# Kernel tuning notes

Measured on AMD Instinct MI355X. Metric: run time of the kernel, lower is better.

The kernel has to match this reference:

```python
import jax, jax.numpy as jnp
import numpy as np

NUM_LAYERS = 12
AGENT_LEN = 10
EMBED = 768
TEXT_DIM = 512
N_TOK = 1024   # h*w patches
BATCH = 32
N_CLS = 150
N_CTX = 77


def setup_inputs() -> dict:
    key = jax.random.key(0)
    ks = jax.random.split(key, 12)
    s = 0.02
    return {
        "output": jax.random.normal(ks[0], (N_TOK + 1, BATCH, EMBED), jnp.float32),
        "text_feat": jax.random.normal(ks[1], (1, N_CLS, N_CTX, TEXT_DIM), jnp.float32),
        "agent": jax.random.uniform(ks[2], (NUM_LAYERS, AGENT_LEN, EMBED), jnp.float32, -0.05, 0.05),
        "agent_scale": jnp.float32(0.001),
        "w1": jax.random.normal(ks[3], (EMBED, EMBED), jnp.float32) * s,
        "b1": jnp.zeros((EMBED,), jnp.float32),
        "w2": jax.random.normal(ks[4], (EMBED, EMBED), jnp.float32) * s,
        "b2": jnp.zeros((EMBED,), jnp.float32),
        "wm": jax.random.normal(ks[5], (EMBED, EMBED), jnp.float32) * s,
        "bm": jnp.zeros((EMBED,), jnp.float32),
        "wt": jax.random.normal(ks[6], (EMBED, TEXT_DIM), jnp.float32) * s,
        "bt": jnp.zeros((EMBED,), jnp.float32),
        "layer": 0,
    }


def _mask_pool(x, m, wm, bm):
    # x: [b, n, d], m: [b, n, a] -> [b, a, d]
    w = jax.nn.sigmoid(m)
    pooled = jnp.einsum('bna,bnd->bad', w, x) / (w.sum(axis=1)[:, :, None] + 1e-6)
    return pooled @ wm.T + bm


def reference(output, text_feat, agent, agent_scale, w1, b1, w2, b2, wm, bm, wt, bt, layer):
    cls_tok, x = output[:1], output[1:]          # [1,b,d], [n,b,d]
    n, b, d = x.shape
    scale = d ** (-0.5)

    # agent tokens for this layer, broadcast to batch
    ag = jnp.broadcast_to(agent[layer], (b, agent.shape[1], d))   # [b,a,d]

    # proj_text: mean over ctx tokens, l2-normalize, linear+relu
    tf = text_feat.mean(axis=-2)                                   # [1,c,text_dim]
    tf = tf / jnp.linalg.norm(tf, axis=-1, keepdims=True)
    temb = jax.nn.relu(tf @ wt.T + bt)                             # [1,c,d]
    temb = jnp.broadcast_to(temb, (b,) + temb.shape[1:])           # [b,c,d]

    feats = x.transpose(1, 0, 2)                                   # [b,n,d]

    # agent_mask
    masked_text = _mask_pool(temb, jnp.einsum('bad,bcd->bca', ag, temb) * scale, wm, bm)
    masked_vis = _mask_pool(feats, jnp.einsum('bnd,bad->bna', feats, ag) * scale, wm, bm)
    ag2 = ag + masked_text + masked_vis                            # [b,a,d]

    # agent_attention: agent <- text
    attn_t = jax.nn.softmax(jnp.einsum('bad,bcd->bac', ag2, temb) * scale, axis=-1)
    v = jnp.einsum('bac,bcd->bad', attn_t, temb) @ w1.T + b1       # [b,a,d]

    # feats <- agent
    attn_v = jax.nn.softmax(jnp.einsum('bnd,bad->bna', feats, ag2) * scale, axis=-1)
    delta = jnp.einsum('bna,bad->bnd', attn_v, v) @ w2.T + b2      # [b,n,d]

    x = x + delta.transpose(1, 0, 2) * agent_scale
    return jnp.concatenate([cls_tok, x], axis=0)
```

## Files before the change

kernel.cpp:

```cpp
#include <hip/hip_runtime.h>
#include <hip/hip_bf16.h>
#include <math.h>

#define BB 32
#define DD 768
#define AL 10
#define NC 150
#define CTX 77
#define TD 512
#define SCALE 0.036084391824351615f
#define CHUNKS 32
#define ROWS_PB 32

__global__ void k_tp1(const float* __restrict__ tfeat, float* __restrict__ tpart) {
    int c = blockIdx.x, qq = blockIdx.y;
    int t = threadIdx.x;
    int j0 = qq * 20, j1 = (qq == 3) ? CTX : j0 + 20;
    const float* base = tfeat + (size_t)c * CTX * TD;
    float s0 = 0.f, s1 = 0.f;
    for (int j = j0; j < j1; ++j) {
        s0 += base[j * TD + t];
        s1 += base[j * TD + t + 256];
    }
    tpart[((size_t)c * 4 + qq) * TD + t] = s0;
    tpart[((size_t)c * 4 + qq) * TD + t + 256] = s1;
}

__global__ void k_tp2(const float* __restrict__ tpart, float* __restrict__ tfn) {
    int c = blockIdx.x, t = threadIdx.x;
    float s0 = 0.f, s1 = 0.f;
    for (int q = 0; q < 4; ++q) {
        s0 += tpart[((size_t)c * 4 + q) * TD + t];
        s1 += tpart[((size_t)c * 4 + q) * TD + t + 256];
    }
    s0 *= (1.f / CTX); s1 *= (1.f / CTX);
    __shared__ float red[256];
    red[t] = s0 * s0 + s1 * s1;
    __syncthreads();
    for (int o = 128; o > 0; o >>= 1) { if (t < o) red[t] += red[t + o]; __syncthreads(); }
    float rn = rsqrtf(red[0]);
    tfn[c * TD + t] = s0 * rn;
    tfn[c * TD + t + 256] = s1 * rn;
}

__global__ void k_temb(const float* __restrict__ tfn, const float* __restrict__ wt,
                       const float* __restrict__ bt, float* __restrict__ temb) {
    int c = blockIdx.x, dch = blockIdx.y;
    int t = threadIdx.x;
    __shared__ float row[TD];
    row[t] = tfn[(size_t)c * TD + t];
    row[t + 256] = tfn[(size_t)c * TD + t + 256];
    __syncthreads();
    int d = dch * 256 + t;
    const float* wr = wt + (size_t)d * TD;
    float acc = bt[d];
    for (int k = 0; k < TD; k += 4) {
        float4 w4 = *reinterpret_cast<const float4*>(wr + k);
        acc += row[k] * w4.x + row[k + 1] * w4.y + row[k + 2] * w4.z + row[k + 3] * w4.w;
    }
    temb[(size_t)c * DD + d] = fmaxf(acc, 0.f);
}

__global__ void k_wtext(const float* __restrict__ temb, const float* __restrict__ agent,
                        const int* __restrict__ layerp, float* __restrict__ wtex) {
    int c = blockIdx.x / AL, a = blockIdx.x % AL;
    int l = threadIdx.x;
    const float* ar = agent + ((size_t)layerp[0] * AL + a) * DD;
    const float* tr = temb + (size_t)c * DD;
    float p = 0.f;
    for (int j = 0; j < 12; ++j) { int d = j * 64 + l; p += ar[d] * tr[d]; }
    #pragma unroll
    for (int o = 1; o < 64; o <<= 1) p += __shfl_xor(p, o);
    if (l == 0) wtex[c * AL + a] = 1.f / (1.f + __expf(-p * SCALE));
}

__global__ void k_ptext(const float* __restrict__ temb, const float* __restrict__ wtex,
                        float* __restrict__ ptex) {
    int a = blockIdx.x / 3, dch = blockIdx.x % 3;
    int d = dch * 256 + threadIdx.x;
    float num = 0.f, den = 0.f;
    for (int c = 0; c < NC; ++c) {
        float wv = wtex[c * AL + a];
        num += wv * temb[(size_t)c * DD + d];
        den += wv;
    }
    ptex[(size_t)a * DD + d] = num / (den + 1e-6f);
}

__global__ void k_mtextB10(const float* __restrict__ ptex, const float* __restrict__ wm,
                           const float* __restrict__ bm, const float* __restrict__ agent,
                           const int* __restrict__ layerp, float* __restrict__ B10) {
    int a = blockIdx.x, dch = blockIdx.y;
    int t = threadIdx.x;
    __shared__ float row[DD];
    for (int i = t; i < DD; i += 256) row[i] = ptex[(size_t)a * DD + i];
    __syncthreads();
    int d = dch * 256 + t;
    const float* wr = wm + (size_t)d * DD;
    float acc = 0.f;
    for (int k = 0; k < DD; k += 4) {
        float4 w4 = *reinterpret_cast<const float4*>(wr + k);
        acc += row[k] * w4.x + row[k + 1] * w4.y + row[k + 2] * w4.z + row[k + 3] * w4.w;
    }
    B10[(size_t)a * DD + d] = acc + bm[d] + agent[((size_t)layerp[0] * AL + a) * DD + d];
}

__global__ __launch_bounds__(256, 2)
void k_pass1(const float* __restrict__ outp, const float* __restrict__ agent,
             const int* __restrict__ layerp, __hip_bfloat16* __restrict__ num_bf,
             float* __restrict__ den_part) {
    int chunk = blockIdx.x, b = blockIdx.y;
    int tid = threadIdx.x, lane = tid & 63, w = tid >> 6;
    __shared__ float agl[AL * DD];
    __shared__ float xs[8][DD];
    __shared__ float wl[ROWS_PB][AL];
    const float* ab = agent + (size_t)layerp[0] * AL * DD;
    for (int i = tid; i < AL * DD; i += 256) agl[i] = ab[i];
    float acc0[AL], acc1[AL], acc2[AL];
    #pragma unroll
    for (int a = 0; a < AL; ++a) { acc0[a] = 0.f; acc1[a] = 0.f; acc2[a] = 0.f; }
    __syncthreads();
    for (int g = 0; g < 4; ++g) {
        int la = w * 2, lb = la + 1;
        int ga = g * 8 + la, gb = ga + 1;
        const float* pA = outp + ((size_t)(1 + chunk * ROWS_PB + ga) * BB + b) * DD + lane * 4;
        const float* pB = pA + (size_t)BB * DD;
        float4 xa0 = *(const float4*)(pA);
        float4 xa1 = *(const float4*)(pA + 256);
        float4 xa2 = *(const float4*)(pA + 512);
        float4 xb0 = *(const float4*)(pB);
        float4 xb1 = *(const float4*)(pB + 256);
        float4 xb2 = *(const float4*)(pB + 512);
        *(float4*)(&xs[la][lane * 4])       = xa0;
        *(float4*)(&xs[la][lane * 4 + 256]) = xa1;
        *(float4*)(&xs[la][lane * 4 + 512]) = xa2;
        *(float4*)(&xs[lb][lane * 4])       = xb0;
        *(float4*)(&xs[lb][lane * 4 + 256]) = xb1;
        *(float4*)(&xs[lb][lane * 4 + 512]) = xb2;
        #pragma unroll
        for (int a = 0; a < AL; ++a) {
            const float* agc = agl + a * DD + lane * 4;
            float4 c0 = *(const float4*)(agc);
            float4 c1 = *(const float4*)(agc + 256);
            float4 c2 = *(const float4*)(agc + 512);
            float pa = xa0.x*c0.x + xa0.y*c0.y + xa0.z*c0.z + xa0.w*c0.w
                     + xa1.x*c1.x + xa1.y*c1.y + xa1.z*c1.z + xa1.w*c1.w
                     + xa2.x*c2.x + xa2.y*c2.y + xa2.z*c2.z + xa2.w*c2.w;
            float pb = xb0.x*c0.x + xb0.y*c0.y + xb0.z*c0.z + xb0.w*c0.w
                     + xb1.x*c1.x + xb1.y*c1.y + xb1.z*c1.z + xb1.w*c1.w
                     + xb2.x*c2.x + xb2.y*c2.y + xb2.z*c2.z + xb2.w*c2.w;
            #pragma unroll
            for (int o = 1; o < 64; o <<= 1) { pa += __shfl_xor(pa, o); pb += __shfl_xor(pb, o); }
            if (lane == a) {
                wl[ga][a] = 1.f / (1.f + __expf(-pa * SCALE));
                wl[gb][a] = 1.f / (1.f + __expf(-pb * SCALE));
            }
        }
        __syncthreads();
        #pragma unroll
        for (int row = 0; row < 8; ++row) {
            float x0 = xs[row][tid], x1 = xs[row][tid + 256], x2 = xs[row][tid + 512];
            int rw = g * 8 + row;
            #pragma unroll
            for (int a = 0; a < AL; ++a) {
                float wg = wl[rw][a];
                acc0[a] += wg * x0; acc1[a] += wg * x1; acc2[a] += wg * x2;
            }
        }
        __syncthreads();
    }
    __hip_bfloat16* np_ = num_bf + ((size_t)b * CHUNKS + chunk) * AL * DD;
    #pragma unroll
    for (int a = 0; a < AL; ++a) {
        np_[a * DD + tid]       = __float2bfloat16(acc0[a]);
        np_[a * DD + tid + 256] = __float2bfloat16(acc1[a]);
        np_[a * DD + tid + 512] = __float2bfloat16(acc2[a]);
    }
    if (tid < AL) {
        float dn = 0.f;
        for (int rw = 0; rw < ROWS_PB; ++rw) dn += wl[rw][tid];
        den_part[((size_t)b * CHUNKS + chunk) * AL + tid] = dn;
    }
}

__global__ void k_poolvis(const __hip_bfloat16* __restrict__ num_bf,
                          const float* __restrict__ den_part, float* __restrict__ pvis) {
    int idx = blockIdx.x;
    int a = idx % AL, b = idx / AL;
    int t = threadIdx.x;
    float den = 0.f;
    for (int c = 0; c < CHUNKS; ++c) den += den_part[((size_t)b * CHUNKS + c) * AL + a];
    float inv = 1.f / (den + 1e-6f);
    for (int dd = 0; dd < 3; ++dd) {
        int d = dd * 256 + t;
        float num = 0.f;
        for (int c = 0; c < CHUNKS; ++c)
            num += __bfloat162float(num_bf[((size_t)b * CHUNKS + c) * AL * DD + a * DD + d]);
        pvis[((size_t)b * AL + a) * DD + d] = num * inv;
    }
}

__global__ __launch_bounds__(256)
void k_gemmsk(const float* __restrict__ A, const float* __restrict__ W,
              float* __restrict__ part) {
    int n0 = blockIdx.x * 64, m0 = blockIdx.y * 64, k0 = blockIdx.z * 192;
    int tid = threadIdx.x;
    int tx = tid % 16, ty = tid / 16;
    __shared__ float As[64][36];
    __shared__ float Ws[64][36];
    float acc[4][4] = {};
    for (int kk = 0; kk < 192; kk += 32) {
        #pragma unroll
        for (int s = 0; s < 2; ++s) {
            int i = s * 256 + tid;
            int r = i >> 3, c4 = (i & 7) * 4;
            float4 av = *reinterpret_cast<const float4*>(A + (size_t)(m0 + r) * DD + k0 + kk + c4);
            float4 wv = *reinterpret_cast<const float4*>(W + (size_t)(n0 + r) * DD + k0 + kk + c4);
            *reinterpret_cast<float4*>(&As[r][c4]) = av;
            *reinterpret_cast<float4*>(&Ws[r][c4]) = wv;
        }
        __syncthreads();
        #pragma unroll
        for (int k4 = 0; k4 < 32; k4 += 4) {
            float4 a[4], wv[4];
            #pragma unroll
            for (int i = 0; i < 4; ++i) a[i] = *reinterpret_cast<const float4*>(&As[ty * 4 + i][k4]);
            #pragma unroll
            for (int j = 0; j < 4; ++j) wv[j] = *reinterpret_cast<const float4*>(&Ws[tx * 4 + j][k4]);
            #pragma unroll
            for (int i = 0; i < 4; ++i)
                #pragma unroll
                for (int j = 0; j < 4; ++j)
                    acc[i][j] += a[i].x * wv[j].x + a[i].y * wv[j].y
                               + a[i].z * wv[j].z + a[i].w * wv[j].w;
        }
        __syncthreads();
    }
    float* pb = part + (size_t)blockIdx.z * 320 * DD;
    #pragma unroll
    for (int i = 0; i < 4; ++i) {
        int m = m0 + ty * 4 + i;
        #pragma unroll
        for (int j = 0; j < 4; ++j)
            pb[(size_t)m * DD + n0 + tx * 4 + j] = acc[i][j];
    }
}

__global__ void k_gemmred(const float* __restrict__ part, const float* __restrict__ bias,
                          const float* __restrict__ brow, float* __restrict__ dst) {
    int m = blockIdx.x, t = threadIdx.x;
    int a = m % AL;
    for (int dd = 0; dd < 3; ++dd) {
        int d = dd * 256 + t;
        float v = part[(size_t)m * DD + d]
                + part[(size_t)320 * DD + (size_t)m * DD + d]
                + part[(size_t)2 * 320 * DD + (size_t)m * DD + d]
                + part[(size_t)3 * 320 * DD + (size_t)m * DD + d];
        v += bias[d];
        if (brow) v += brow[(size_t)a * DD + d];
        dst[(size_t)m * DD + d] = v;
    }
}

__global__ void k_tattn(const float* __restrict__ ag2, const float* __restrict__ temb,
                        float* __restrict__ u) {
    int a = blockIdx.x, b = blockIdx.y;
    int t = threadIdx.x;
    __shared__ float q[DD];
    __shared__ float p[NC];
    __shared__ float red[256];
    const float* qb = ag2 + ((size_t)b * AL + a) * DD;
    for (int i = t; i < DD; i += 256) q[i] = qb[i];
    __syncthreads();
    float myp = -1e30f;
    if (t < NC) {
        const float* tr = temb + (size_t)t * DD;
        float s = 0.f;
        for (int k = 0; k < DD; k += 4) {
            float4 t4 = *reinterpret_cast<const float4*>(tr + k);
            s += q[k] * t4.x + q[k + 1] * t4.y + q[k + 2] * t4.z + q[k + 3] * t4.w;
        }
        myp = s * SCALE;
    }
    red[t] = myp; __syncthreads();
    for (int o = 128; o > 0; o >>= 1) { if (t < o) red[t] = fmaxf(red[t], red[t + o]); __syncthreads(); }
    float mx = red[0]; __syncthreads();
    float e = (t < NC) ? __expf(myp - mx) : 0.f;
    red[t] = e; __syncthreads();
    for (int o = 128; o > 0; o >>= 1) { if (t < o) red[t] += red[t + o]; __syncthreads(); }
    float inv = 1.f / red[0];
    if (t < NC) p[t] = e * inv;
    __syncthreads();
    float u0 = 0.f, u1 = 0.f, u2 = 0.f;
    for (int c = 0; c < NC; ++c) {
        const float* tr = temb + (size_t)c * DD;
        float pc = p[c];
        u0 += pc * tr[t]; u1 += pc * tr[t + 256]; u2 += pc * tr[t + 512];
    }
    float* ur = u + ((size_t)b * AL + a) * DD;
    ur[t] = u0; ur[t + 256] = u1; ur[t + 512] = u2;
}

__global__ __launch_bounds__(256, 2)
void k_pass2(const float* __restrict__ outp, const float* __restrict__ ag2,
             const float* __restrict__ v2, const float* __restrict__ ascale,
             float* __restrict__ out) {
    int chunk = blockIdx.x, b = blockIdx.y;
    int tid = threadIdx.x, lane = tid & 63, w = tid >> 6;
    __shared__ float agl[AL * DD];
    __shared__ float xs[8][DD];
    __shared__ float pl[8][AL];
    float vr0[AL], vr1[AL], vr2[AL];
    #pragma unroll
    for (int a = 0; a < AL; ++a) {
        const float* vrow = v2 + ((size_t)b * AL + a) * DD;
        vr0[a] = vrow[tid]; vr1[a] = vrow[tid + 256]; vr2[a] = vrow[tid + 512];
    }
    const float* ab = ag2 + (size_t)b * AL * DD;
    for (int i = tid; i < AL * DD; i += 256) agl[i] = ab[i];
    float asc = ascale[0];
    __syncthreads();
    for (int g = 0; g < 4; ++g) {
        int la = w * 2, lb = la + 1;
        int ga = g * 8 + la, gb = ga + 1;
        const float* pA = outp + ((size_t)(1 + chunk * ROWS_PB + ga) * BB + b) * DD + lane * 4;
        const float* pB = pA + (size_t)BB * DD;
        float4 xa0 = *(const float4*)(pA);
        float4 xa1 = *(const float4*)(pA + 256);
        float4 xa2 = *(const float4*)(pA + 512);
        float4 xb0 = *(const float4*)(pB);
        float4 xb1 = *(const float4*)(pB + 256);
        float4 xb2 = *(const float4*)(pB + 512);
        *(float4*)(&xs[la][lane * 4])       = xa0;
        *(float4*)(&xs[la][lane * 4 + 256]) = xa1;
        *(float4*)(&xs[la][lane * 4 + 512]) = xa2;
        *(float4*)(&xs[lb][lane * 4])       = xb0;
        *(float4*)(&xs[lb][lane * 4 + 256]) = xb1;
        *(float4*)(&xs[lb][lane * 4 + 512]) = xb2;
        float sA[AL], sB[AL];
        #pragma unroll
        for (int a = 0; a < AL; ++a) {
            const float* agc = agl + a * DD + lane * 4;
            float4 c0 = *(const float4*)(agc);
            float4 c1 = *(const float4*)(agc + 256);
            float4 c2 = *(const float4*)(agc + 512);
            float pa = xa0.x*c0.x + xa0.y*c0.y + xa0.z*c0.z + xa0.w*c0.w
                     + xa1.x*c1.x + xa1.y*c1.y + xa1.z*c1.z + xa1.w*c1.w
                     + xa2.x*c2.x + xa2.y*c2.y + xa2.z*c2.z + xa2.w*c2.w;
            float pb = xb0.x*c0.x + xb0.y*c0.y + xb0.z*c0.z + xb0.w*c0.w
                     + xb1.x*c1.x + xb1.y*c1.y + xb1.z*c1.z + xb1.w*c1.w
                     + xb2.x*c2.x + xb2.y*c2.y + xb2.z*c2.z + xb2.w*c2.w;
            #pragma unroll
            for (int o = 1; o < 64; o <<= 1) { pa += __shfl_xor(pa, o); pb += __shfl_xor(pb, o); }
            sA[a] = pa * SCALE; sB[a] = pb * SCALE;
        }
        float mA = sA[0], mB = sB[0];
        #pragma unroll
        for (int a = 1; a < AL; ++a) { mA = fmaxf(mA, sA[a]); mB = fmaxf(mB, sB[a]); }
        float ZA = 0.f, ZB = 0.f;
        #pragma unroll
        for (int a = 0; a < AL; ++a) {
            sA[a] = __expf(sA[a] - mA); ZA += sA[a];
            sB[a] = __expf(sB[a] - mB); ZB += sB[a];
        }
        float iA = asc / ZA, iB = asc / ZB;
        #pragma unroll
        for (int a = 0; a < AL; ++a) {
            if (lane == a) { pl[la][a] = sA[a] * iA; pl[lb][a] = sB[a] * iB; }
        }
        __syncthreads();
        #pragma unroll
        for (int row = 0; row < 8; ++row) {
            float x0 = xs[row][tid], x1 = xs[row][tid + 256], x2 = xs[row][tid + 512];
            float d0 = 0.f, d1 = 0.f, d2 = 0.f;
            #pragma unroll
            for (int a = 0; a < AL; ++a) {
                float pa = pl[row][a];
                d0 += pa * vr0[a]; d1 += pa * vr1[a]; d2 += pa * vr2[a];
            }
            float* orow = out + ((size_t)(1 + chunk * ROWS_PB + g * 8 + row) * BB + b) * DD;
            orow[tid]       = x0 + d0;
            orow[tid + 256] = x1 + d1;
            orow[tid + 512] = x2 + d2;
        }
        __syncthreads();
    }
}

extern "C" void kernel_launch(void* const* d_in, const int* in_sizes, int n_in,
                              void* d_out, int out_size, void* d_ws, size_t ws_size,
                              hipStream_t stream) {
    const float* outp   = (const float*)d_in[0];
    const float* tfeat  = (const float*)d_in[1];
    const float* agent  = (const float*)d_in[2];
    const float* ascale = (const float*)d_in[3];
    const float* w1 = (const float*)d_in[4];
    const float* b1 = (const float*)d_in[5];
    const float* w2 = (const float*)d_in[6];
    const float* b2 = (const float*)d_in[7];
    const float* wm = (const float*)d_in[8];
    const float* bm = (const float*)d_in[9];
    const float* wt = (const float*)d_in[10];
    const float* bt = (const float*)d_in[11];
    const int* layerp = (const int*)d_in[12];
    float* out = (float*)d_out;

    float* ws = (float*)d_ws;
    float* tfn   = ws;
    float* temb  = tfn + NC * TD;
    float* wtex  = temb + NC * DD;
    float* ptex  = wtex + NC * AL;
    float* B10   = ptex + AL * DD;
    float* pvis  = B10 + AL * DD;
    float* ag2   = pvis + BB * AL * DD;
    float* u     = ag2 + BB * AL * DD;
    float* v     = u + BB * AL * DD;
    float* v2    = v + BB * AL * DD;
    float* den_part = v2 + BB * AL * DD;
    __hip_bfloat16* num_bf = (__hip_bfloat16*)(den_part + BB * CHUNKS * AL);
    float* tpart = u;
    float* part  = (float*)num_bf;

    hipMemcpyAsync(out, outp, (size_t)BB * DD * sizeof(float),
                   hipMemcpyDeviceToDevice, stream);

    k_pass1<<<dim3(CHUNKS, BB), 256, 0, stream>>>(outp, agent, layerp, num_bf, den_part);
    k_tp1<<<dim3(NC, 4), 256, 0, stream>>>(tfeat, tpart);
    k_tp2<<<NC, 256, 0, stream>>>(tpart, tfn);
    k_temb<<<dim3(NC, 3), 256, 0, stream>>>(tfn, wt, bt, temb);
    k_wtext<<<NC * AL, 64, 0, stream>>>(temb, agent, layerp, wtex);
    k_ptext<<<30, 256, 0, stream>>>(temb, wtex, ptex);
    k_mtextB10<<<dim3(AL, 3), 256, 0, stream>>>(ptex, wm, bm, agent, layerp, B10);
    k_poolvis<<<BB * AL, 256, 0, stream>>>(num_bf, den_part, pvis);
    k_gemmsk<<<dim3(12, 5, 4), 256, 0, stream>>>(pvis, wm, part);
    k_gemmred<<<320, 256, 0, stream>>>(part, bm, B10, ag2);
    k_tattn<<<dim3(AL, BB), 256, 0, stream>>>(ag2, temb, u);
    k_gemmsk<<<dim3(12, 5, 4), 256, 0, stream>>>(u, w1, part);
    k_gemmred<<<320, 256, 0, stream>>>(part, b1, nullptr, v);
    k_gemmsk<<<dim3(12, 5, 4), 256, 0, stream>>>(v, w2, part);
    k_gemmred<<<320, 256, 0, stream>>>(part, b2, nullptr, v2);
    k_pass2<<<dim3(CHUNKS, BB), 256, 0, stream>>>(outp, ag2, v2, ascale, out);
}
```

Measured before the change: 478.9 us.

## Fuse text-path kernels, fold split-K reductions into consumers, drop smem staging in passes

The text projection path is collapsed from six kernels to three: the split context sum is merged into one kernel, the agent-text dot products are fused into the temb projection via shared and global atomics, and pooling is fused with the wm GEMV. The separate split-K reduction kernels are removed; consumers (tattn, pass2, and a new GEMM that sums partials plus bias while loading A) add the four partial slices directly. k_pass1 and k_pass2 no longer stage rows in shared memory, re-reading x from global in a second loop, and their occupancy hint rises from 2 to 4. This cuts launches and intermediate traffic but re-reads the large activation tensor and duplicates partial-sum work across blocks.

```diff
diff --git a/kernel.cpp b/kernel.cpp
--- a/kernel.cpp
+++ b/kernel.cpp
@@ -11,27 +11,16 @@
 #define SCALE 0.036084391824351615f
 #define CHUNKS 32
 #define ROWS_PB 32
-
-__global__ void k_tp1(const float* __restrict__ tfeat, float* __restrict__ tpart) {
-    int c = blockIdx.x, qq = blockIdx.y;
-    int t = threadIdx.x;
-    int j0 = qq * 20, j1 = (qq == 3) ? CTX : j0 + 20;
+#define PS ((size_t)320 * DD)
+
+__global__ void k_tp(const float* __restrict__ tfeat, float* __restrict__ tfn) {
+    int c = blockIdx.x, t = threadIdx.x;
     const float* base = tfeat + (size_t)c * CTX * TD;
     float s0 = 0.f, s1 = 0.f;
-    for (int j = j0; j < j1; ++j) {
+    #pragma unroll 4
+    for (int j = 0; j < CTX; ++j) {
         s0 += base[j * TD + t];
         s1 += base[j * TD + t + 256];
-    }
-    tpart[((size_t)c * 4 + qq) * TD + t] = s0;
-    tpart[((size_t)c * 4 + qq) * TD + t + 256] = s1;
-}
-
-__global__ void k_tp2(const float* __restrict__ tpart, float* __restrict__ tfn) {
-    int c = blockIdx.x, t = threadIdx.x;
-    float s0 = 0.f, s1 = 0.f;
-    for (int q = 0; q < 4; ++q) {
-        s0 += tpart[((size_t)c * 4 + q) * TD + t];
-        s1 += tpart[((size_t)c * 4 + q) * TD + t + 256];
     }
     s0 *= (1.f / CTX); s1 *= (1.f / CTX);
     __shared__ float red[256];
@@ -44,12 +33,16 @@
 }
 
 __global__ void k_temb(const float* __restrict__ tfn, const float* __restrict__ wt,
-                       const float* __restrict__ bt, float* __restrict__ temb) {
+                       const float* __restrict__ bt, const float* __restrict__ agent,
+                       const int* __restrict__ layerp, float* __restrict__ temb,
+                       float* __restrict__ wtex_raw) {
     int c = blockIdx.x, dch = blockIdx.y;
-    int t = threadIdx.x;
+    int t = threadIdx.x, lane = t & 63;
     __shared__ float row[TD];
+    __shared__ float wsum[16];
     row[t] = tfn[(size_t)c * TD + t];
     row[t + 256] = tfn[(size_t)c * TD + t + 256];
+    if (t < 16) wsum[t] = 0.f;
     __syncthreads();
     int d = dch * 256 + t;
     const float* wr = wt + (size_t)d * TD;
@@ -58,72 +51,70 @@
         float4 w4 = *reinterpret_cast<const float4*>(wr + k);
         acc += row[k] * w4.x + row[k + 1] * w4.y + row[k + 2] * w4.z + row[k + 3] * w4.w;
     }
-    temb[(size_t)c * DD + d] = fmaxf(acc, 0.f);
-}
-
-__global__ void k_wtext(const float* __restrict__ temb, const float* __restrict__ agent,
-                        const int* __restrict__ layerp, float* __restrict__ wtex) {
-    int c = blockIdx.x / AL, a = blockIdx.x % AL;
-    int l = threadIdx.x;
-    const float* ar = agent + ((size_t)layerp[0] * AL + a) * DD;
-    const float* tr = temb + (size_t)c * DD;
-    float p = 0.f;
-    for (int j = 0; j < 12; ++j) { int d = j * 64 + l; p += ar[d] * tr[d]; }
-    #pragma unroll
-    for (int o = 1; o < 64; o <<= 1) p += __shfl_xor(p, o);
-    if (l == 0) wtex[c * AL + a] = 1.f / (1.f + __expf(-p * SCALE));
-}
-
-__global__ void k_ptext(const float* __restrict__ temb, const float* __restrict__ wtex,
-                        float* __restrict__ ptex) {
-    int a = blockIdx.x / 3, dch = blockIdx.x % 3;
-    int d = dch * 256 + threadIdx.x;
-    float num = 0.f, den = 0.f;
-    for (int c = 0; c < NC; ++c) {
-        float wv = wtex[c * AL + a];
-        num += wv * temb[(size_t)c * DD + d];
-        den += wv;
-    }
-    ptex[(size_t)a * DD + d] = num / (den + 1e-6f);
-}
-
-__global__ void k_mtextB10(const float* __restrict__ ptex, const float* __restrict__ wm,
-                           const float* __restrict__ bm, const float* __restrict__ agent,
-                           const int* __restrict__ layerp, float* __restrict__ B10) {
+    float tv = fmaxf(acc, 0.f);
+    temb[(size_t)c * DD + d] = tv;
+    const float* ag = agent + (size_t)layerp[0] * AL * DD + d;
+    #pragma unroll
+    for (int a = 0; a < AL; ++a) {
+        float p = tv * ag[(size_t)a * DD];
+        #pragma unroll
+        for (int o = 1; o < 64; o <<= 1) p += __shfl_xor(p, o);
+        if (lane == 0) atomicAdd(&wsum[a], p);
+    }
+    __syncthreads();
+    if (t < AL) atomicAdd(&wtex_raw[c * AL + t], wsum[t]);
+}
+
+__global__ void k_text2(const float* __restrict__ temb, const float* __restrict__ wtex_raw,
+                        const float* __restrict__ wm, const float* __restrict__ bm,
+                        const float* __restrict__ agent, const int* __restrict__ layerp,
+                        float* __restrict__ B10) {
     int a = blockIdx.x, dch = blockIdx.y;
     int t = threadIdx.x;
-    __shared__ float row[DD];
-    for (int i = t; i < DD; i += 256) row[i] = ptex[(size_t)a * DD + i];
+    __shared__ float pooled[DD];
+    __shared__ float wv[NC];
+    __shared__ float red[256];
+    float myw = 0.f;
+    if (t < NC) { myw = 1.f / (1.f + __expf(-wtex_raw[t * AL + a] * SCALE)); wv[t] = myw; }
+    red[t] = myw;
+    __syncthreads();
+    for (int o = 128; o > 0; o >>= 1) { if (t < o) red[t] += red[t + o]; __syncthreads(); }
+    float inv = 1.f / (red[0] + 1e-6f);
+    float p0 = 0.f, p1 = 0.f, p2 = 0.f;
+    #pragma unroll 2
+    for (int c = 0; c < NC; ++c) {
+        float wc = wv[c];
+        const float* tr = temb + (size_t)c * DD;
+        p0 += wc * tr[t]; p1 += wc * tr[t + 256]; p2 += wc * tr[t + 512];
+    }
+    pooled[t] = p0 * inv; pooled[t + 256] = p1 * inv; pooled[t + 512] = p2 * inv;
     __syncthreads();
     int d = dch * 256 + t;
     const float* wr = wm + (size_t)d * DD;
     float acc = 0.f;
     for (int k = 0; k < DD; k += 4) {
         float4 w4 = *reinterpret_cast<const float4*>(wr + k);
-        acc += row[k] * w4.x + row[k + 1] * w4.y + row[k + 2] * w4.z + row[k + 3] * w4.w;
+        acc += pooled[k] * w4.x + pooled[k + 1] * w4.y + pooled[k + 2] * w4.z + pooled[k + 3] * w4.w;
     }
     B10[(size_t)a * DD + d] = acc + bm[d] + agent[((size_t)layerp[0] * AL + a) * DD + d];
 }
 
-__global__ __launch_bounds__(256, 2)
+__global__ __launch_bounds__(256, 4)
 void k_pass1(const float* __restrict__ outp, const float* __restrict__ agent,
              const int* __restrict__ layerp, __hip_bfloat16* __restrict__ num_bf,
              float* __restrict__ den_part) {
     int chunk = blockIdx.x, b = blockIdx.y;
     int tid = threadIdx.x, lane = tid & 63, w = tid >> 6;
     __shared__ float agl[AL * DD];
-    __shared__ float xs[8][DD];
     __shared__ float wl[ROWS_PB][AL];
     const float* ab = agent + (size_t)layerp[0] * AL * DD;
     for (int i = tid; i < AL * DD; i += 256) agl[i] = ab[i];
-    float acc0[AL], acc1[AL], acc2[AL];
-    #pragma unroll
-    for (int a = 0; a < AL; ++a) { acc0[a] = 0.f; acc1[a] = 0.f; acc2[a] = 0.f; }
-    __syncthreads();
-    for (int g = 0; g < 4; ++g) {
-        int la = w * 2, lb = la + 1;
-        int ga = g * 8 + la, gb = ga + 1;
-        const float* pA = outp + ((size_t)(1 + chunk * ROWS_PB + ga) * BB + b) * DD + lane * 4;
+    __syncthreads();
+    const float4* agl4 = reinterpret_cast<const float4*>(agl);
+    #pragma unroll
+    for (int pr = 0; pr < 4; ++pr) {
+        int ra = w * 8 + pr * 2, rb = ra + 1;
+        const float* pA = outp + ((size_t)(1 + chunk * ROWS_PB + ra) * BB + b) * DD + lane * 4;
         const float* pB = pA + (size_t)BB * DD;
         float4 xa0 = *(const float4*)(pA);
         float4 xa1 = *(const float4*)(pA + 256);
@@ -131,18 +122,11 @@
         float4 xb0 = *(const float4*)(pB);
         float4 xb1 = *(const float4*)(pB + 256);
         float4 xb2 = *(const float4*)(pB + 512);
-        *(float4*)(&xs[la][lane * 4])       = xa0;
-        *(float4*)(&xs[la][lane * 4 + 256]) = xa1;
-        *(float4*)(&xs[la][lane * 4 + 512]) = xa2;
-        *(float4*)(&xs[lb][lane * 4])       = xb0;
-        *(float4*)(&xs[lb][lane * 4 + 256]) = xb1;
-        *(float4*)(&xs[lb][lane * 4 + 512]) = xb2;
-        #pragma unroll
-        for (int a = 0; a < AL; ++a) {
-            const float* agc = agl + a * DD + lane * 4;
-            float4 c0 = *(const float4*)(agc);
-            float4 c1 = *(const float4*)(agc + 256);
-            float4 c2 = *(const float4*)(agc + 512);
+        #pragma unroll
+        for (int a = 0; a < AL; ++a) {
+            float4 c0 = agl4[a * 192 + lane];
+            float4 c1 = agl4[a * 192 + 64 + lane];
+            float4 c2 = agl4[a * 192 + 128 + lane];
             float pa = xa0.x*c0.x + xa0.y*c0.y + xa0.z*c0.z + xa0.w*c0.w
                      + xa1.x*c1.x + xa1.y*c1.y + xa1.z*c1.z + xa1.w*c1.w
                      + xa2.x*c2.x + xa2.y*c2.y + xa2.z*c2.z + xa2.w*c2.w;
@@ -152,22 +136,24 @@
             #pragma unroll
             for (int o = 1; o < 64; o <<= 1) { pa += __shfl_xor(pa, o); pb += __shfl_xor(pb, o); }
             if (lane == a) {
-                wl[ga][a] = 1.f / (1.f + __expf(-pa * SCALE));
-                wl[gb][a] = 1.f / (1.f + __expf(-pb * SCALE));
+                wl[ra][a] = 1.f / (1.f + __expf(-pa * SCALE));
+                wl[rb][a] = 1.f / (1.f + __expf(-pb * SCALE));
             }
         }
-        __syncthreads();
-        #pragma unroll
-        for (int row = 0; row < 8; ++row) {
-            float x0 = xs[row][tid], x1 = xs[row][tid + 256], x2 = xs[row][tid + 512];
-            int rw = g * 8 + row;
-            #pragma unroll
-            for (int a = 0; a < AL; ++a) {
-                float wg = wl[rw][a];
-                acc0[a] += wg * x0; acc1[a] += wg * x1; acc2[a] += wg * x2;
-            }
-        }
-        __syncthreads();
+    }
+    __syncthreads();
+    float acc0[AL], acc1[AL], acc2[AL];
+    #pragma unroll
+    for (int a = 0; a < AL; ++a) { acc0[a] = 0.f; acc1[a] = 0.f; acc2[a] = 0.f; }
+    #pragma unroll 4
+    for (int row = 0; row < ROWS_PB; ++row) {
+        const float* fr = outp + ((size_t)(1 + chunk * ROWS_PB + row) * BB + b) * DD;
+        float x0 = fr[tid], x1 = fr[tid + 256], x2 = fr[tid + 512];
+        #pragma unroll
+        for (int a = 0; a < AL; ++a) {
+            float wg = wl[row][a];
+            acc0[a] += wg * x0; acc1[a] += wg * x1; acc2[a] += wg * x2;
+        }
     }
     __hip_bfloat16* np_ = num_bf + ((size_t)b * CHUNKS + chunk) * AL * DD;
     #pragma unroll
@@ -178,6 +164,7 @@
     }
     if (tid < AL) {
         float dn = 0.f;
+        #pragma unroll
         for (int rw = 0; rw < ROWS_PB; ++rw) dn += wl[rw][tid];
         den_part[((size_t)b * CHUNKS + chunk) * AL + tid] = dn;
     }
@@ -194,6 +181,7 @@
     for (int dd = 0; dd < 3; ++dd) {
         int d = dd * 256 + t;
         float num = 0.f;
+        #pragma unroll 4
         for (int c = 0; c < CHUNKS; ++c)
             num += __bfloat162float(num_bf[((size_t)b * CHUNKS + c) * AL * DD + a * DD + d]);
         pvis[((size_t)b * AL + a) * DD + d] = num * inv;
@@ -236,7 +224,7 @@
         }
         __syncthreads();
     }
-    float* pb = part + (size_t)blockIdx.z * 320 * DD;
+    float* pb = part + (size_t)blockIdx.z * PS;
     #pragma unroll
     for (int i = 0; i < 4; ++i) {
         int m = m0 + ty * 4 + i;
@@ -246,31 +234,74 @@
     }
 }
 
-__global__ void k_gemmred(const float* __restrict__ part, const float* __restrict__ bias,
-                          const float* __restrict__ brow, float* __restrict__ dst) {
-    int m = blockIdx.x, t = threadIdx.x;
-    int a = m % AL;
-    for (int dd = 0; dd < 3; ++dd) {
-        int d = dd * 256 + t;
-        float v = part[(size_t)m * DD + d]
-                + part[(size_t)320 * DD + (size_t)m * DD + d]
-                + part[(size_t)2 * 320 * DD + (size_t)m * DD + d]
-                + part[(size_t)3 * 320 * DD + (size_t)m * DD + d];
-        v += bias[d];
-        if (brow) v += brow[(size_t)a * DD + d];
-        dst[(size_t)m * DD + d] = v;
-    }
-}
-
-__global__ void k_tattn(const float* __restrict__ ag2, const float* __restrict__ temb,
+__global__ __launch_bounds__(256)
+void k_gemmskf(const float* __restrict__ Aparts, const float* __restrict__ kbias,
+               const float* __restrict__ W, float* __restrict__ part) {
+    int n0 = blockIdx.x * 64, m0 = blockIdx.y * 64, k0 = blockIdx.z * 192;
+    int tid = threadIdx.x;
+    int tx = tid % 16, ty = tid / 16;
+    __shared__ float As[64][36];
+    __shared__ float Ws[64][36];
+    float acc[4][4] = {};
+    for (int kk = 0; kk < 192; kk += 32) {
+        #pragma unroll
+        for (int s = 0; s < 2; ++s) {
+            int i = s * 256 + tid;
+            int r = i >> 3, c4 = (i & 7) * 4;
+            size_t aoff = (size_t)(m0 + r) * DD + k0 + kk + c4;
+            float4 a0 = *reinterpret_cast<const float4*>(Aparts + aoff);
+            float4 a1 = *reinterpret_cast<const float4*>(Aparts + PS + aoff);
+            float4 a2 = *reinterpret_cast<const float4*>(Aparts + 2 * PS + aoff);
+            float4 a3 = *reinterpret_cast<const float4*>(Aparts + 3 * PS + aoff);
+            float4 bb = *reinterpret_cast<const float4*>(kbias + k0 + kk + c4);
+            float4 av;
+            av.x = a0.x + a1.x + a2.x + a3.x + bb.x;
+            av.y = a0.y + a1.y + a2.y + a3.y + bb.y;
+            av.z = a0.z + a1.z + a2.z + a3.z + bb.z;
+            av.w = a0.w + a1.w + a2.w + a3.w + bb.w;
+            float4 wv = *reinterpret_cast<const float4*>(W + (size_t)(n0 + r) * DD + k0 + kk + c4);
+            *reinterpret_cast<float4*>(&As[r][c4]) = av;
+            *reinterpret_cast<float4*>(&Ws[r][c4]) = wv;
+        }
+        __syncthreads();
+        #pragma unroll
+        for (int k4 = 0; k4 < 32; k4 += 4) {
+            float4 a[4], wv[4];
+            #pragma unroll
+            for (int i = 0; i < 4; ++i) a[i] = *reinterpret_cast<const float4*>(&As[ty * 4 + i][k4]);
+            #pragma unroll
+            for (int j = 0; j < 4; ++j) wv[j] = *reinterpret_cast<const float4*>(&Ws[tx * 4 + j][k4]);
+            #pragma unroll
+            for (int i = 0; i < 4; ++i)
+                #pragma unroll
+                for (int j = 0; j < 4; ++j)
+                    acc[i][j] += a[i].x * wv[j].x + a[i].y * wv[j].y
+                               + a[i].z * wv[j].z + a[i].w * wv[j].w;
+        }
+        __syncthreads();
+    }
+    float* pb = part + (size_t)blockIdx.z * PS;
+    #pragma unroll
+    for (int i = 0; i < 4; ++i) {
+        int m = m0 + ty * 4 + i;
+        #pragma unroll
+        for (int j = 0; j < 4; ++j)
+            pb[(size_t)m * DD + n0 + tx * 4 + j] = acc[i][j];
+    }
+}
+
+__global__ void k_tattn(const float* __restrict__ partsA, const float* __restrict__ bm,
+                        const float* __restrict__ B10, const float* __restrict__ temb,
                         float* __restrict__ u) {
     int a = blockIdx.x, b = blockIdx.y;
     int t = threadIdx.x;
     __shared__ float q[DD];
     __shared__ float p[NC];
     __shared__ float red[256];
-    const float* qb = ag2 + ((size_t)b * AL + a) * DD;
-    for (int i = t; i < DD; i += 256) q[i] = qb[i];
+    const float* pA = partsA + ((size_t)b * AL + a) * DD;
+    const float* br = B10 + (size_t)a * DD;
+    for (int i = t; i < DD; i += 256)
+        q[i] = pA[i] + pA[PS + i] + pA[2 * PS + i] + pA[3 * PS + i] + bm[i] + br[i];
     __syncthreads();
     float myp = -1e30f;
     if (t < NC) {
@@ -292,6 +323,7 @@
     if (t < NC) p[t] = e * inv;
     __syncthreads();
     float u0 = 0.f, u1 = 0.f, u2 = 0.f;
+    #pragma unroll 2
     for (int c = 0; c < NC; ++c) {
         const float* tr = temb + (size_t)c * DD;
         float pc = p[c];
@@ -301,49 +333,53 @@
     ur[t] = u0; ur[t + 256] = u1; ur[t + 512] = u2;
 }
 
-__global__ __launch_bounds__(256, 2)
-void k_pass2(const float* __restrict__ outp, const float* __restrict__ ag2,
-             const float* __restrict__ v2, const float* __restrict__ ascale,
-             float* __restrict__ out) {
+__global__ __launch_bounds__(256, 4)
+void k_pass2(const float* __restrict__ outp, const float* __restrict__ partsA,
+             const float* __restrict__ bm, const float* __restrict__ B10,
+             const float* __restrict__ partsC, const float* __restrict__ b2,
+             const float* __restrict__ ascale, float* __restrict__ out) {
     int chunk = blockIdx.x, b = blockIdx.y;
     int tid = threadIdx.x, lane = tid & 63, w = tid >> 6;
     __shared__ float agl[AL * DD];
-    __shared__ float xs[8][DD];
-    __shared__ float pl[8][AL];
+    __shared__ float pl[ROWS_PB][AL];
     float vr0[AL], vr1[AL], vr2[AL];
+    const float* pC = partsC + (size_t)b * AL * DD;
     #pragma unroll
     for (int a = 0; a < AL; ++a) {
-        const float* vrow = v2 + ((size_t)b * AL + a) * DD;
-        vr0[a] = vrow[tid]; vr1[a] = vrow[tid + 256]; vr2[a] = vrow[tid + 512];
-    }
-    const float* ab = ag2 + (size_t)b * AL * DD;
-    for (int i = tid; i < AL * DD; i += 256) agl[i] = ab[i];
+        size_t i0 = (size_t)a * DD + tid;
+        vr0[a] = pC[i0] + pC[PS + i0] + pC[2 * PS + i0] + pC[3 * PS + i0] + b2[tid];
+        size_t i1 = i0 + 256;
+        vr1[a] = pC[i1] + pC[PS + i1] + pC[2 * PS + i1] + pC[3 * PS + i1] + b2[tid + 256];
+        size_t i2 = i0 + 512;
+        vr2[a] = pC[i2] + pC[PS + i2] + pC[2 * PS + i2] + pC[3 * PS + i2] + b2[tid + 512];
+    }
+    const float* pA = partsA + (size_t)b * AL * DD;
+    #pragma unroll
+    for (int j = 0; j < 30; ++j) {
+        int a = j / 3, d = (j % 3) * 256 + tid;
+        int i = a * DD + d;
+        agl[i] = pA[i] + pA[PS + i] + pA[2 * PS + i] + pA[3 * PS + i] + bm[d] + B10[i];
+    }
     float asc = ascale[0];
     __syncthreads();
-    for (int g = 0; g < 4; ++g) {
-        int la = w * 2, lb = la + 1;
-        int ga = g * 8 + la, gb = ga + 1;
-        const float* pA = outp + ((size_t)(1 + chunk * ROWS_PB + ga) * BB + b) * DD + lane * 4;
-        const float* pB = pA + (size_t)BB * DD;
-        float4 xa0 = *(const float4*)(pA);
-        float4 xa1 = *(const float4*)(pA + 256);
-        float4 xa2 = *(const float4*)(pA + 512);
-        float4 xb0 = *(const float4*)(pB);
-        float4 xb1 = *(const float4*)(pB + 256);
-        float4 xb2 = *(const float4*)(pB + 512);
-        *(float4*)(&xs[la][lane * 4])       = xa0;
-        *(float4*)(&xs[la][lane * 4 + 256]) = xa1;
-        *(float4*)(&xs[la][lane * 4 + 512]) = xa2;
-        *(float4*)(&xs[lb][lane * 4])       = xb0;
-        *(float4*)(&xs[lb][lane * 4 + 256]) = xb1;
-        *(float4*)(&xs[lb][lane * 4 + 512]) = xb2;
+    const float4* agl4 = reinterpret_cast<const float4*>(agl);
+    #pragma unroll
+    for (int pr = 0; pr < 4; ++pr) {
+        int ra = w * 8 + pr * 2, rb = ra + 1;
+        const float* pAx = outp + ((size_t)(1 + chunk * ROWS_PB + ra) * BB + b) * DD + lane * 4;
+        const float* pBx = pAx + (size_t)BB * DD;
+        float4 xa0 = *(const float4*)(pAx);
+        float4 xa1 = *(const float4*)(pAx + 256);
+        float4 xa2 = *(const float4*)(pAx + 512);
+        float4 xb0 = *(const float4*)(pBx);
+        float4 xb1 = *(const float4*)(pBx + 256);
+        float4 xb2 = *(const float4*)(pBx + 512);
         float sA[AL], sB[AL];
         #pragma unroll
         for (int a = 0; a < AL; ++a) {
-            const float* agc = agl + a * DD + lane * 4;
-            float4 c0 = *(const float4*)(agc);
-            float4 c1 = *(const float4*)(agc + 256);
-            float4 c2 = *(const float4*)(agc + 512);
+            float4 c0 = agl4[a * 192 + lane];
+            float4 c1 = agl4[a * 192 + 64 + lane];
+            float4 c2 = agl4[a * 192 + 128 + lane];
             float pa = xa0.x*c0.x + xa0.y*c0.y + xa0.z*c0.z + xa0.w*c0.w
                      + xa1.x*c1.x + xa1.y*c1.y + xa1.z*c1.z + xa1.w*c1.w
                      + xa2.x*c2.x + xa2.y*c2.y + xa2.z*c2.z + xa2.w*c2.w;
@@ -366,24 +402,24 @@
         float iA = asc / ZA, iB = asc / ZB;
         #pragma unroll
         for (int a = 0; a < AL; ++a) {
-            if (lane == a) { pl[la][a] = sA[a] * iA; pl[lb][a] = sB[a] * iB; }
-        }
-        __syncthreads();
-        #pragma unroll
-        for (int row = 0; row < 8; ++row) {
-            float x0 = xs[row][tid], x1 = xs[row][tid + 256], x2 = xs[row][tid + 512];
-            float d0 = 0.f, d1 = 0.f, d2 = 0.f;
-            #pragma unroll
-            for (int a = 0; a < AL; ++a) {
-                float pa = pl[row][a];
-                d0 += pa * vr0[a]; d1 += pa * vr1[a]; d2 += pa * vr2[a];
-            }
-            float* orow = out + ((size_t)(1 + chunk * ROWS_PB + g * 8 + row) * BB + b) * DD;
-            orow[tid]       = x0 + d0;
-            orow[tid + 256] = x1 + d1;
-            orow[tid + 512] = x2 + d2;
-        }
-        __syncthreads();
+            if (lane == a) { pl[ra][a] = sA[a] * iA; pl[rb][a] = sB[a] * iB; }
+        }
+    }
+    __syncthreads();
+    #pragma unroll 4
+    for (int row = 0; row < ROWS_PB; ++row) {
+        const float* fr = outp + ((size_t)(1 + chunk * ROWS_PB + row) * BB + b) * DD;
+        float x0 = fr[tid], x1 = fr[tid + 256], x2 = fr[tid + 512];
+        float d0 = 0.f, d1 = 0.f, d2 = 0.f;
+        #pragma unroll
+        for (int a = 0; a < AL; ++a) {
+            float pa = pl[row][a];
+            d0 += pa * vr0[a]; d1 += pa * vr1[a]; d2 += pa * vr2[a];
+        }
+        float* orow = out + ((size_t)(1 + chunk * ROWS_PB + row) * BB + b) * DD;
+        orow[tid]       = x0 + d0;
+        orow[tid + 256] = x1 + d1;
+        orow[tid + 512] = x2 + d2;
     }
 }
 
@@ -406,38 +442,31 @@
     float* out = (float*)d_out;
 
     float* ws = (float*)d_ws;
-    float* tfn   = ws;
-    float* temb  = tfn + NC * TD;
-    float* wtex  = temb + NC * DD;
-    float* ptex  = wtex + NC * AL;
-    float* B10   = ptex + AL * DD;
-    float* pvis  = B10 + AL * DD;
-    float* ag2   = pvis + BB * AL * DD;
-    float* u     = ag2 + BB * AL * DD;
-    float* v     = u + BB * AL * DD;
-    float* v2    = v + BB * AL * DD;
-    float* den_part = v2 + BB * AL * DD;
-    __hip_bfloat16* num_bf = (__hip_bfloat16*)(den_part + BB * CHUNKS * AL);
-    float* tpart = u;
-    float* part  = (float*)num_bf;
-
+    float* tfn      = ws;
+    float* temb     = tfn + 76800;
+    float* wtex_raw = temb + 115200;
+    float* B10      = wtex_raw + 1536;
+    float* pvis     = B10 + 7680;
+    float* u        = pvis + 245760;
+    float* den_part = u + 245760;
+    float* big      = den_part + 10240;
+    float* partsA = big;
+    float* partsB = big + 983040;
+    float* partsC = big + 1966080;
+    __hip_bfloat16* num_bf = (__hip_bfloat16*)big;
+
+    hipMemsetAsync(wtex_raw, 0, NC * AL * sizeof(float), stream);
     hipMemcpyAsync(out, outp, (size_t)BB * DD * sizeof(float),
                    hipMemcpyDeviceToDevice, stream);
 
     k_pass1<<<dim3(CHUNKS, BB), 256, 0, stream>>>(outp, agent, layerp, num_bf, den_part);
-    k_tp1<<<dim3(NC, 4), 256, 0, stream>>>(tfeat, tpart);
-    k_tp2<<<NC, 256, 0, stream>>>(tpart, tfn);
-    k_temb<<<dim3(NC, 3), 256, 0, stream>>>(tfn, wt, bt, temb);
-    k_wtext<<<NC * AL, 64, 0, stream>>>(temb, agent, layerp, wtex);
-    k_ptext<<<30, 256, 0, stream>>>(temb, wtex, ptex);
-    k_mtextB10<<<dim3(AL, 3), 256, 0, stream>>>(ptex, wm, bm, agent, layerp, B10);
+    k_tp<<<NC, 256, 0, stream>>>(tfeat, tfn);
+    k_temb<<<dim3(NC, 3), 256, 0, stream>>>(tfn, wt, bt, agent, layerp, temb, wtex_raw);
+    k_text2<<<dim3(AL, 3), 256, 0, stream>>>(temb, wtex_raw, wm, bm, agent, layerp, B10);
     k_poolvis<<<BB * AL, 256, 0, stream>>>(num_bf, den_part, pvis);
-    k_gemmsk<<<dim3(12, 5, 4), 256, 0, stream>>>(pvis, wm, part);
-    k_gemmred<<<320, 256, 0, stream>>>(part, bm, B10, ag2);
-    k_tattn<<<dim3(AL, BB), 256, 0, stream>>>(ag2, temb, u);
-    k_gemmsk<<<dim3(12, 5, 4), 256, 0, stream>>>(u, w1, part);
-    k_gemmred<<<320, 256, 0, stream>>>(part, b1, nullptr, v);
-    k_gemmsk<<<dim3(12, 5, 4), 256, 0, stream>>>(v, w2, part);
-    k_gemmred<<<320, 256, 0, stream>>>(part, b2, nullptr, v2);
-    k_pass2<<<dim3(CHUNKS, BB), 256, 0, stream>>>(outp, ag2, v2, ascale, out);
-}
+    k_gemmsk<<<dim3(12, 5, 4), 256, 0, stream>>>(pvis, wm, partsA);
+    k_tattn<<<dim3(AL, BB), 256, 0, stream>>>(partsA, bm, B10, temb, u);
+    k_gemmsk<<<dim3(12, 5, 4), 256, 0, stream>>>(u, w1, partsB);
+    k_gemmskf<<<dim3(12, 5, 4), 256, 0, stream>>>(partsB, b1, w2, partsC);
+    k_pass2<<<dim3(CHUNKS, BB), 256, 0, stream>>>(outp, partsA, bm, B10, partsC, b2, ascale, out);
+}
```

After: 554.6 us. +15.8%, slower.
